# Performance work log

Hardware: AMD Instinct MI355X
Metric: run time of the kernel (lower is better)

The kernel has to match this reference:

```python
import jax, jax.numpy as jnp
import numpy as np

B, S, N_EMBD = 4, 4096, 1024
HIDDEN = 4 * N_EMBD
M_BITS_FC = 3
M_BITS_PROJ = 3
BLOCK_K = 32


def block_quant(v, m_bits, bk):
    """Block-floating-point quantization along the last (K) dim.
    Each block of `bk` elements shares an exponent derived from its max-abs;
    mantissas are rounded to `m_bits` bits. Straight-through estimator for grads."""
    *lead, K = v.shape
    vb = v.reshape(*lead, K // bk, bk)
    amax = jnp.max(jnp.abs(vb), axis=-1, keepdims=True)
    tiny = jnp.asarray(2.0 ** -126, v.dtype)
    e = jnp.floor(jnp.log2(jnp.maximum(amax, tiny)))  # shared block exponent
    scale = jnp.exp2(e - m_bits)                       # quantization step
    q = jnp.round(vb / scale) * scale
    q = vb + jax.lax.stop_gradient(q - vb)             # STE
    return q.reshape(v.shape)


def lowprec_linear(x, w, b, m_bits, bk):
    # w: [out, in]; quantize both operands along the contraction dim.
    xq = block_quant(x, m_bits, bk)
    wq = block_quant(w, m_bits, bk)
    return jnp.einsum('bsk,nk->bsn', xq, wq) + b


def setup_inputs() -> dict:
    key = jax.random.key(0)
    k0, k1, k2 = jax.random.split(key, 3)
    x = jax.random.normal(k0, (B, S, N_EMBD), jnp.float32)
    w_fc = jax.random.normal(k1, (HIDDEN, N_EMBD), jnp.float32) * (1.0 / np.sqrt(N_EMBD))
    b_fc = jnp.zeros((HIDDEN,), jnp.float32)
    w_proj = jax.random.normal(k2, (N_EMBD, HIDDEN), jnp.float32) * (1.0 / np.sqrt(HIDDEN))
    b_proj = jnp.zeros((N_EMBD,), jnp.float32)
    return {"x": x, "w_fc": w_fc, "b_fc": b_fc, "w_proj": w_proj, "b_proj": b_proj}


def reference(x, w_fc, b_fc, w_proj, b_proj):
    h = lowprec_linear(x, w_fc, b_fc, M_BITS_FC, BLOCK_K)
    h = jax.nn.gelu(h, approximate=False)  # nn.GELU default = exact erf
    return lowprec_linear(h, w_proj, b_proj, M_BITS_PROJ, BLOCK_K)
```

## Files before the change

kernel.cpp:

```cpp
#include <hip/hip_runtime.h>
#include <hip/hip_bf16.h>

using bf16 = __hip_bfloat16;
typedef __attribute__((ext_vector_type(8))) short short8;
typedef __attribute__((ext_vector_type(4))) float f32x4;

#define DI __device__ __forceinline__

constexpr int MROWS = 16384;
constexpr int EMB   = 1024;
constexpr int HID   = 4096;

DI void gload16(const bf16* g, bf16* l) {
  __builtin_amdgcn_global_load_lds((const __attribute__((address_space(1))) void*)g,
                                   (__attribute__((address_space(3))) void*)l,
                                   16, 0, 0);
}

DI void qparams(float amax, float& scale, float& inv) {
  int eb = (int)((__float_as_uint(amax) >> 23) & 255u);
  eb = eb < 4 ? 4 : eb;
  scale = __uint_as_float((unsigned)(eb - 3) << 23);
  inv   = __uint_as_float((unsigned)(257 - eb) << 23);
}

__global__ void quant32(const float* __restrict__ in, bf16* __restrict__ out, int nblk) {
  int b = blockIdx.x * blockDim.x + threadIdx.x;
  if (b >= nblk) return;
  const float4* p = (const float4*)(in + (size_t)b * 32);
  float4 v[8];
  float amax = 0.f;
#pragma unroll
  for (int i = 0; i < 8; i++) {
    v[i] = p[i];
    amax = fmaxf(amax, fmaxf(fmaxf(fabsf(v[i].x), fabsf(v[i].y)),
                             fmaxf(fabsf(v[i].z), fabsf(v[i].w))));
  }
  float scale, inv;
  qparams(amax, scale, inv);
  alignas(16) unsigned short us[32];
#pragma unroll
  for (int i = 0; i < 8; i++) {
    us[i * 4 + 0] = (unsigned short)(__float_as_uint(rintf(v[i].x * inv) * scale) >> 16);
    us[i * 4 + 1] = (unsigned short)(__float_as_uint(rintf(v[i].y * inv) * scale) >> 16);
    us[i * 4 + 2] = (unsigned short)(__float_as_uint(rintf(v[i].z * inv) * scale) >> 16);
    us[i * 4 + 3] = (unsigned short)(__float_as_uint(rintf(v[i].w * inv) * scale) >> 16);
  }
  short8* o = (short8*)(out + (size_t)b * 32);
#pragma unroll
  for (int i = 0; i < 4; i++) o[i] = *(short8*)(us + i * 8);
}

#define MFMA16(a, b, c) __builtin_amdgcn_mfma_f32_16x16x32_bf16(a, b, c, 0, 0, 0)
#define SBAR()    __builtin_amdgcn_s_barrier()
#define WAITVM(n) asm volatile("s_waitcnt vmcnt(" #n ")" ::: "memory")

#define Q_MFMA(MB, NB, BG) \
  __builtin_amdgcn_s_setprio(1); \
  _Pragma("unroll") for (int kk = 0; kk < 2; kk++) \
  _Pragma("unroll") for (int mi = 0; mi < 4; mi++) \
  _Pragma("unroll") for (int ni = 0; ni < 2; ni++) \
    acc[(MB) + mi][(NB) + ni] = MFMA16(af[mi * 2 + kk], BG[ni * 2 + kk], acc[(MB) + mi][(NB) + ni]); \
  __builtin_amdgcn_s_setprio(0);

#define RD_AF(mh) \
  _Pragma("unroll") for (int mi = 0; mi < 4; mi++) { \
    af[mi * 2]     = ldA(db, mh, mi, 0); \
    af[mi * 2 + 1] = ldA(db, mh, mi, 1); }

#define RD_B(half, dst) \
  _Pragma("unroll") for (int ni = 0; ni < 2; ni++) { \
    dst[ni * 2]     = ldB(db, half, ni, 0); \
    dst[ni * 2 + 1] = ldB(db, half, ni, 1); }

template<int Kd, int Nd, bool GQ>
__global__ void __launch_bounds__(512, 2)
gemm8(const bf16* __restrict__ Ap, const bf16* __restrict__ Bp,
      const float* __restrict__ bias, void* __restrict__ Cout) {
  __shared__ alignas(16) bf16 SH[65536];
  bf16* Abuf = SH;
  bf16* Bbuf = SH + 32768;

  const int tid  = threadIdx.x;
  const int lane = tid & 63, wave = tid >> 6;
  const int l16  = lane & 15, lhi = lane >> 4;
  const int wr   = wave >> 2, wc  = wave & 3;

  const int idx  = blockIdx.x >> 3;
  const int xid  = blockIdx.x & 7;
  const int brow = (xid * 8 + (idx & 7)) * 256;
  const int bcol = (idx >> 3) * 256;

  const int r0 = tid >> 3;
  const int sl = (tid & 7) ^ (r0 & 7);
  const bf16* asrc = Ap + (size_t)(brow + r0) * Kd + sl * 8;
  const bf16* bsrc = Bp + (size_t)(bcol + r0) * Kd + sl * 8;

  auto stA = [&](int tt, int half) {
    const bf16* s = asrc + (size_t)half * 128 * Kd + tt * 64;
    bf16* d = Abuf + ((tt & 1) * 2 + half) * 8192 + tid * 8;
    gload16(s, d); gload16(s + (size_t)64 * Kd, d + 4096);
  };
  auto stB = [&](int tt, int half) {
    const bf16* s = bsrc + (size_t)half * 128 * Kd + tt * 64;
    bf16* d = Bbuf + ((tt & 1) * 2 + half) * 8192 + tid * 8;
    gload16(s, d); gload16(s + (size_t)64 * Kd, d + 4096);
  };

  const int sx = l16 & 7;
  const int arow = wr * 16 + l16;
  auto ldA = [&](int db, int mh, int mi, int kk) -> short8 {
    return *(const short8*)(Abuf + (db * 2 + mh) * 8192 +
                            (mi * 32 + arow) * 64 + ((kk * 4 + lhi) ^ sx) * 8);
  };
  const int brl = wc * 32 + l16;
  auto ldB = [&](int db, int half, int ni, int kk) -> short8 {
    return *(const short8*)(Bbuf + (db * 2 + half) * 8192 +
                            (brl + ni * 16) * 64 + ((kk * 4 + lhi) ^ sx) * 8);
  };

  f32x4 acc[8][4] = {};
  short8 af[8], bgl[4], bgh[4];

  constexpr int NT = Kd / 64;

  stA(0, 0); stB(0, 0); stB(0, 1); stA(0, 1);
  stA(1, 0); stB(1, 0); stB(1, 1);
  WAITVM(6); SBAR();

  for (int t = 0; t <= NT - 3; ++t) {
    const int db = t & 1;
    RD_AF(0) RD_B(0, bgl) RD_B(1, bgh)
    stA(t + 1, 1);
    Q_MFMA(0, 0, bgl)
    stA(t + 2, 0);
    Q_MFMA(0, 2, bgh)
    stB(t + 2, 0);
    RD_AF(1)
    stB(t + 2, 1);
    Q_MFMA(4, 0, bgl)
    Q_MFMA(4, 2, bgh)
    WAITVM(6); SBAR();
  }

  {
    const int db = (NT - 2) & 1;
    RD_AF(0) RD_B(0, bgl) RD_B(1, bgh)
    stA(NT - 1, 1);
    Q_MFMA(0, 0, bgl)
    Q_MFMA(0, 2, bgh)
    RD_AF(1)
    Q_MFMA(4, 0, bgl)
    Q_MFMA(4, 2, bgh)
    WAITVM(0); SBAR();
  }

  {
    const int db = (NT - 1) & 1;
    RD_AF(0) RD_B(0, bgl) RD_B(1, bgh)
    Q_MFMA(0, 0, bgl)
    Q_MFMA(0, 2, bgh)
    RD_AF(1)
    Q_MFMA(4, 0, bgl)
    Q_MFMA(4, 2, bgh)
  }

  const int cb = bcol + wc * 32;
  float bv[4];
#pragma unroll
  for (int n = 0; n < 4; n++) bv[n] = bias[cb + (n >> 1) * 128 + (n & 1) * 16 + l16];

  if constexpr (GQ) {
    SBAR();
#pragma unroll
    for (int m = 0; m < 8; m++) {
      const int rl0 = m * 32 + wr * 16 + lhi * 4;
#pragma unroll
      for (int r = 0; r < 4; r++) {
        float g[4];
#pragma unroll
        for (int n = 0; n < 4; n++) {
          float v = acc[m][n][r] + bv[n];
          g[n] = 0.5f * v * (1.0f + erff(v * 0.70710678118654752f));
        }
#pragma unroll
        for (int p = 0; p < 2; p++) {
          float am = fmaxf(fabsf(g[p * 2]), fabsf(g[p * 2 + 1]));
#pragma unroll
          for (int msk = 1; msk <= 8; msk <<= 1) am = fmaxf(am, __shfl_xor(am, msk, 64));
          float sc, iv; qparams(am, sc, iv);
          const int rowb = (rl0 + r) * 256;
          const int c0   = wc * 32 + p * 128;
          SH[rowb + ((c0 + l16)      ^ (lhi << 3))] = __float2bfloat16(rintf(g[p * 2]     * iv) * sc);
          SH[rowb + ((c0 + 16 + l16) ^ (lhi << 3))] = __float2bfloat16(rintf(g[p * 2 + 1] * iv) * sc);
        }
      }
    }
    SBAR();
    bf16* outp = (bf16*)Cout;
#pragma unroll
    for (int i = 0; i < 16; i++) {
      const int c   = i * 512 + tid;
      const int row = c >> 5, cc = c & 31;
      const int scc = cc ^ ((row >> 2) & 3);
      *(short8*)(outp + (size_t)(brow + row) * Nd + bcol + cc * 8) =
          *(const short8*)(SH + (size_t)row * 256 + scc * 8);
    }
  } else {
    float* outp = (float*)Cout;
#pragma unroll
    for (int m = 0; m < 8; m++) {
      const size_t rbase = (size_t)(brow + m * 32 + wr * 16 + lhi * 4);
#pragma unroll
      for (int r = 0; r < 4; r++) {
        const size_t ro = (rbase + r) * Nd;
#pragma unroll
        for (int n = 0; n < 4; n++)
          outp[ro + cb + (n >> 1) * 128 + (n & 1) * 16 + l16] = acc[m][n][r] + bv[n];
      }
    }
  }
}

extern "C" void kernel_launch(void* const* d_in, const int* in_sizes, int n_in,
                              void* d_out, int out_size, void* d_ws, size_t ws_size,
                              hipStream_t stream) {
  const float* x      = (const float*)d_in[0];
  const float* w_fc   = (const float*)d_in[1];
  const float* b_fc   = (const float*)d_in[2];
  const float* w_proj = (const float*)d_in[3];
  const float* b_proj = (const float*)d_in[4];

  char* ws = (char*)d_ws;
  bf16* xq  = (bf16*)ws;  ws += (size_t)MROWS * EMB * 2;
  bf16* wfq = (bf16*)ws;  ws += (size_t)HID * EMB * 2;
  bf16* wpq = (bf16*)ws;  ws += (size_t)EMB * HID * 2;
  bf16* hq  = (bf16*)ws;

  quant32<<<(MROWS * EMB / 32 + 255) / 256, 256, 0, stream>>>(x, xq, MROWS * EMB / 32);
  quant32<<<(HID * EMB / 32 + 255) / 256, 256, 0, stream>>>(w_fc, wfq, HID * EMB / 32);
  quant32<<<(EMB * HID / 32 + 255) / 256, 256, 0, stream>>>(w_proj, wpq, EMB * HID / 32);

  gemm8<EMB, HID, true ><<<(MROWS / 256) * (HID / 256), 512, 0, stream>>>(xq, wfq, b_fc, hq);
  gemm8<HID, EMB, false><<<(MROWS / 256) * (EMB / 256), 512, 0, stream>>>(hq, wpq, b_proj, (float*)d_out);
}
```

Before: 344.9 us.

## Unfuse GELU+quant epilogue into separate kernel when workspace allows; add nontemporal loads/stores

When the workspace is large enough, the first GEMM now writes fp32 pre-activations to a new 256 MB buffer. A separate grid-stride kernel then applies exact GELU and the 32-wide block quantization, with amax reduced by lane shuffles across 8 lanes. This removes the LDS staging, barriers and erf work from the GEMM epilogue, but adds a large fp32 write and read of the hidden tensor through HBM. Nontemporal loads in quant32 and nontemporal stores in the output epilogue are added to limit cache pollution.

New measurement: 367.6 us. +6.6%, slower.

```diff
diff --git a/kernel.cpp b/kernel.cpp
--- a/kernel.cpp
+++ b/kernel.cpp
@@ -4,6 +4,7 @@
 using bf16 = __hip_bfloat16;
 typedef __attribute__((ext_vector_type(8))) short short8;
 typedef __attribute__((ext_vector_type(4))) float f32x4;
+typedef __attribute__((ext_vector_type(4))) unsigned short u16x4;
 
 #define DI __device__ __forceinline__
 
@@ -27,28 +28,48 @@
 __global__ void quant32(const float* __restrict__ in, bf16* __restrict__ out, int nblk) {
   int b = blockIdx.x * blockDim.x + threadIdx.x;
   if (b >= nblk) return;
-  const float4* p = (const float4*)(in + (size_t)b * 32);
-  float4 v[8];
+  const f32x4* p = (const f32x4*)(in + (size_t)b * 32);
+  f32x4 v[8];
   float amax = 0.f;
 #pragma unroll
   for (int i = 0; i < 8; i++) {
-    v[i] = p[i];
-    amax = fmaxf(amax, fmaxf(fmaxf(fabsf(v[i].x), fabsf(v[i].y)),
-                             fmaxf(fabsf(v[i].z), fabsf(v[i].w))));
+    v[i] = __builtin_nontemporal_load(p + i);
+    amax = fmaxf(amax, fmaxf(fmaxf(fabsf(v[i][0]), fabsf(v[i][1])),
+                             fmaxf(fabsf(v[i][2]), fabsf(v[i][3]))));
   }
   float scale, inv;
   qparams(amax, scale, inv);
   alignas(16) unsigned short us[32];
 #pragma unroll
-  for (int i = 0; i < 8; i++) {
-    us[i * 4 + 0] = (unsigned short)(__float_as_uint(rintf(v[i].x * inv) * scale) >> 16);
-    us[i * 4 + 1] = (unsigned short)(__float_as_uint(rintf(v[i].y * inv) * scale) >> 16);
-    us[i * 4 + 2] = (unsigned short)(__float_as_uint(rintf(v[i].z * inv) * scale) >> 16);
-    us[i * 4 + 3] = (unsigned short)(__float_as_uint(rintf(v[i].w * inv) * scale) >> 16);
-  }
+  for (int i = 0; i < 8; i++)
+#pragma unroll
+    for (int j = 0; j < 4; j++)
+      us[i * 4 + j] = (unsigned short)(__float_as_uint(rintf(v[i][j] * inv) * scale) >> 16);
   short8* o = (short8*)(out + (size_t)b * 32);
 #pragma unroll
   for (int i = 0; i < 4; i++) o[i] = *(short8*)(us + i * 8);
+}
+
+__global__ void gelu_quant(const float* __restrict__ h, bf16* __restrict__ out, int n4) {
+  const int stride = gridDim.x * blockDim.x;
+  for (int i = blockIdx.x * blockDim.x + threadIdx.x; i < n4; i += stride) {
+    f32x4 v = __builtin_nontemporal_load((const f32x4*)h + i);
+    float g[4];
+#pragma unroll
+    for (int j = 0; j < 4; j++)
+      g[j] = 0.5f * v[j] * (1.0f + erff(v[j] * 0.70710678118654752f));
+    float am = fmaxf(fmaxf(fabsf(g[0]), fabsf(g[1])), fmaxf(fabsf(g[2]), fabsf(g[3])));
+    am = fmaxf(am, __shfl_xor(am, 1, 64));
+    am = fmaxf(am, __shfl_xor(am, 2, 64));
+    am = fmaxf(am, __shfl_xor(am, 4, 64));
+    float sc, iv;
+    qparams(am, sc, iv);
+    u16x4 u;
+#pragma unroll
+    for (int j = 0; j < 4; j++)
+      u[j] = (unsigned short)(__float_as_uint(rintf(g[j] * iv) * sc) >> 16);
+    *(u16x4*)((unsigned short*)out + (size_t)i * 4) = u;
+  }
 }
 
 #define MFMA16(a, b, c) __builtin_amdgcn_mfma_f32_16x16x32_bf16(a, b, c, 0, 0, 0)
@@ -216,7 +237,8 @@
         const size_t ro = (rbase + r) * Nd;
 #pragma unroll
         for (int n = 0; n < 4; n++)
-          outp[ro + cb + (n >> 1) * 128 + (n & 1) * 16 + l16] = acc[m][n][r] + bv[n];
+          __builtin_nontemporal_store(acc[m][n][r] + bv[n],
+              &outp[ro + cb + (n >> 1) * 128 + (n & 1) * 16 + l16]);
       }
     }
   }
@@ -231,16 +253,35 @@
   const float* w_proj = (const float*)d_in[3];
   const float* b_proj = (const float*)d_in[4];
 
-  char* ws = (char*)d_ws;
-  bf16* xq  = (bf16*)ws;  ws += (size_t)MROWS * EMB * 2;
-  bf16* wfq = (bf16*)ws;  ws += (size_t)HID * EMB * 2;
-  bf16* wpq = (bf16*)ws;  ws += (size_t)EMB * HID * 2;
-  bf16* hq  = (bf16*)ws;
-
-  quant32<<<(MROWS * EMB / 32 + 255) / 256, 256, 0, stream>>>(x, xq, MROWS * EMB / 32);
-  quant32<<<(HID * EMB / 32 + 255) / 256, 256, 0, stream>>>(w_fc, wfq, HID * EMB / 32);
-  quant32<<<(EMB * HID / 32 + 255) / 256, 256, 0, stream>>>(w_proj, wpq, EMB * HID / 32);
-
-  gemm8<EMB, HID, true ><<<(MROWS / 256) * (HID / 256), 512, 0, stream>>>(xq, wfq, b_fc, hq);
-  gemm8<HID, EMB, false><<<(MROWS / 256) * (EMB / 256), 512, 0, stream>>>(hq, wpq, b_proj, (float*)d_out);
-}
+  char* base = (char*)d_ws;
+  const size_t MB = 1u << 20;
+
+  if (ws_size >= 392 * MB) {
+    bf16*  wpq = (bf16*)(base);
+    bf16*  xq  = (bf16*)(base + 8 * MB);
+    bf16*  wfq = (bf16*)(base + 40 * MB);
+    bf16*  hq  = (bf16*)(base + 8 * MB);
+    float* h   = (float*)(base + 136 * MB);
+
+    quant32<<<(MROWS * EMB / 32 + 255) / 256, 256, 0, stream>>>(x, xq, MROWS * EMB / 32);
+    quant32<<<(HID * EMB / 32 + 255) / 256, 256, 0, stream>>>(w_fc, wfq, HID * EMB / 32);
+    quant32<<<(EMB * HID / 32 + 255) / 256, 256, 0, stream>>>(w_proj, wpq, EMB * HID / 32);
+
+    gemm8<EMB, HID, false><<<(MROWS / 256) * (HID / 256), 512, 0, stream>>>(xq, wfq, b_fc, h);
+    gelu_quant<<<2048, 256, 0, stream>>>(h, hq, MROWS * HID / 4);
+    gemm8<HID, EMB, false><<<(MROWS / 256) * (EMB / 256), 512, 0, stream>>>(hq, wpq, b_proj, (float*)d_out);
+  } else {
+    char* ws = base;
+    bf16* xq  = (bf16*)ws;  ws += (size_t)MROWS * EMB * 2;
+    bf16* wfq = (bf16*)ws;  ws += (size_t)HID * EMB * 2;
+    bf16* wpq = (bf16*)ws;  ws += (size_t)EMB * HID * 2;
+    bf16* hq  = (bf16*)ws;
+
+    quant32<<<(MROWS * EMB / 32 + 255) / 256, 256, 0, stream>>>(x, xq, MROWS * EMB / 32);
+    quant32<<<(HID * EMB / 32 + 255) / 256, 256, 0, stream>>>(w_fc, wfq, HID * EMB / 32);
+    quant32<<<(EMB * HID / 32 + 255) / 256, 256, 0, stream>>>(w_proj, wpq, EMB * HID / 32);
+
+    gemm8<EMB, HID, true ><<<(MROWS / 256) * (HID / 256), 512, 0, stream>>>(xq, wfq, b_fc, hq);
+    gemm8<HID, EMB, false><<<(MROWS / 256) * (EMB / 256), 512, 0, stream>>>(hq, wpq, b_proj, (float*)d_out);
+  }
+}
```
